# Optimization experiments

Hardware: AMD Instinct MI355X
Metric: run time of the kernel (lower is better)

## Reference

```python
import jax, jax.numpy as jnp
import numpy as np

DN = ('NCHW', 'OIHW', 'NCHW')  # data, weight, output layouts


def conv3x3(x, w):
    # stride 1, padding 1 -> spatial dims preserved (matches MyConv2d kernel_size=3, padding=1)
    return jax.lax.conv_general_dilated(
        x, w, window_strides=(1, 1), padding=((1, 1), (1, 1)), dimension_numbers=DN)


def setup_inputs() -> dict:
    key = jax.random.key(0)
    kx, k1, k2, k3 = jax.random.split(key, 4)
    N, Cin, Cmid, Cout, H, W = 16, 64, 128, 64, 224, 224
    x = jax.random.normal(kx, (N, Cin, H, W), dtype=jnp.float32)
    # Kaiming-like scaling: std = 1/sqrt(fan_in) keeps activations well-conditioned
    w1 = jax.random.normal(k1, (Cmid, Cin, 3, 3), dtype=jnp.float32) / np.sqrt(Cin * 9)
    w2 = jax.random.normal(k2, (Cmid, Cmid, 3, 3), dtype=jnp.float32) / np.sqrt(Cmid * 9)
    w3 = jax.random.normal(k3, (Cout, Cmid, 3, 3), dtype=jnp.float32) / np.sqrt(Cmid * 9)
    return {"x": x, "w1": w1, "w2": w2, "w3": w3}


def reference(x, w1, w2, w3):
    # MyNet.forward: conv1 -> conv2 -> conv3 (no bias, no activation in source)
    x = conv3x3(x, w1)
    x = conv3x3(x, w2)
    return conv3x3(x, w3)
```

## Files before the change

### kernel.cpp

```cpp
#include <hip/hip_runtime.h>
#include <hip/hip_bf16.h>

typedef __attribute__((ext_vector_type(8))) short short8;
typedef __attribute__((ext_vector_type(4))) float f32x4;
typedef __attribute__((ext_vector_type(4))) int   i32x4;
typedef __hip_bfloat16 bf16_t;

#define HH 224
#define WW 224
#define HWSZ (224*224)
#define NIMG 16

template<int CIN>
__global__ __launch_bounds__(256)
void prep_x(const float* __restrict__ x, bf16_t* __restrict__ xc) {
  constexpr int NCC = CIN/32;
  __shared__ float tile[32][225];
  int b = blockIdx.x;
  int cc = b % NCC; int h = (b/NCC) % HH; int n = b / (NCC*HH);
  const float* src = x + ((long)(n*CIN + cc*32))*HWSZ + (long)h*WW;
  for (int i = threadIdx.x; i < 32*WW; i += 256) {
    int ci = i / WW, w = i - ci*WW;
    tile[ci][w] = src[(long)ci*HWSZ + w];
  }
  __syncthreads();
  bf16_t* dst = xc + ((long)(n*HH + h)*NCC + cc)*(WW*32);
  for (int i = threadIdx.x; i < WW*32; i += 256) {
    int w = i >> 5, ci = i & 31;
    dst[i] = __float2bfloat16(tile[ci][w]);
  }
}

__global__ __launch_bounds__(256)
void prep_w(const float* __restrict__ w, bf16_t* __restrict__ wb, int Cout, int Cin) {
  int idx = blockIdx.x*256 + threadIdx.x;
  if (idx >= 9*Cout*Cin) return;
  int ci = idx % Cin; int r = idx / Cin; int co = r % Cout; int t = r / Cout;
  wb[idx] = __float2bfloat16(w[((long)co*Cin + ci)*9 + t]);
}

template<int CIN, int COUT, bool FINAL>
__global__ __launch_bounds__(256, 2)
void conv3x3(const bf16_t* __restrict__ in, const bf16_t* __restrict__ wb,
             void* __restrict__ outp)
{
  constexpr int NCC = CIN/32;
  __shared__ unsigned short lds_x[4*226*32];

  const int tid  = threadIdx.x;
  const int lane = tid & 63;
  const int l15  = lane & 15;
  const int lk   = lane >> 4;
  const int wv   = tid >> 6;
  const int rw   = wv >> 1;
  const int cb   = (wv & 1)*112;

  const int tile = blockIdx.x;
  const int n    = tile / 112;
  const int h0   = (tile - n*112)*2;
  const int co0  = blockIdx.y * 64;

  f32x4 acc[7][4];
  #pragma unroll
  for (int m=0;m<7;++m)
    #pragma unroll
    for (int q=0;q<4;++q) acc[m][q] = (f32x4){0.f,0.f,0.f,0.f};

  const bf16_t* inb   = in + (long)n * ((long)HH*NCC*WW*32);
  const bf16_t* wlane = wb + (long)(co0 + l15)*CIN + lk*8;

  for (int c = 0; c < NCC; ++c) {
    __syncthreads();
    #pragma unroll
    for (int i = 0; i < 4; ++i) {
      int hh = h0 - 1 + i;
      const char* rowp = (const char*)(inb + ((long)hh*NCC + c)*(WW*32));
      bool rowok = (hh >= 0) & (hh < HH);
      for (int off = tid*16; off < 226*64; off += 256*16) {
        int j = off >> 6;
        int wcol = j - 1;
        i32x4 v = (i32x4){0,0,0,0};
        if (rowok && (unsigned)wcol < (unsigned)WW)
          v = *(const i32x4*)(rowp + wcol*64 + (off & 63));
        int a = i*14464 + off;
        a ^= ((a>>7)&3)<<4;
        *(i32x4*)((char*)lds_x + a) = v;
      }
    }
    const bf16_t* wc = wlane + c*32;
    short8 bf[4];
    #pragma unroll
    for (int q=0;q<4;++q)
      bf[q] = *(const short8*)(wc + (long)(q*16)*CIN);
    __syncthreads();

    for (int t = 0; t < 9; ++t) {
      short8 bfn[4];
      if (t < 8) {
        #pragma unroll
        for (int q=0;q<4;++q)
          bfn[q] = *(const short8*)(wc + (long)((t+1)*COUT + q*16)*CIN);
      }
      const int dh = t/3, dw = t - (t/3)*3;
      const int arow = (rw + dh)*226;
      #pragma unroll
      for (int m=0;m<7;++m) {
        int a = (arow + cb + m*16 + l15 + dw)*64 + lk*16;
        a ^= ((a>>7)&3)<<4;
        short8 af = *(const short8*)((const char*)lds_x + a);
        #pragma unroll
        for (int q=0;q<4;++q)
          acc[m][q] = __builtin_amdgcn_mfma_f32_16x16x32_bf16(af, bf[q], acc[m][q], 0,0,0);
      }
      if (t < 8) {
        #pragma unroll
        for (int q=0;q<4;++q) bf[q] = bfn[q];
      }
    }
  }

  const int orow = h0 + rw;
  if (!FINAL) {
    bf16_t* out = (bf16_t*)outp;
    long ob = ((long)(n*HH + orow)*(COUT/32))*(WW*32);
    #pragma unroll
    for (int m=0;m<7;++m) {
      #pragma unroll
      for (int q=0;q<4;++q) {
        int co = co0 + q*16 + l15;
        long base = ob + ((long)(co>>5)*WW)*32 + (co & 31);
        int col = cb + m*16 + lk*4;
        #pragma unroll
        for (int jj=0;jj<4;++jj)
          out[base + (long)(col+jj)*32] = __float2bfloat16(acc[m][q][jj]);
      }
    }
  } else {
    float* out = (float*)outp;
    #pragma unroll
    for (int m=0;m<7;++m) {
      #pragma unroll
      for (int q=0;q<4;++q) {
        int co = co0 + q*16 + l15;
        int col = cb + m*16 + lk*4;
        *(f32x4*)(out + ((long)(n*COUT + co)*HH + orow)*WW + col) = acc[m][q];
      }
    }
  }
}

extern "C" void kernel_launch(void* const* d_in, const int* in_sizes, int n_in,
                              void* d_out, int out_size, void* d_ws, size_t ws_size,
                              hipStream_t stream) {
  (void)in_sizes; (void)n_in; (void)out_size; (void)ws_size;
  const float* x  = (const float*)d_in[0];
  const float* w1 = (const float*)d_in[1];
  const float* w2 = (const float*)d_in[2];
  const float* w3 = (const float*)d_in[3];

  const size_t SB = (size_t)NIMG*HH*WW*128*2;
  char* ws = (char*)d_ws;
  bf16_t* bufA = (bf16_t*)ws;
  bf16_t* a1   = (bf16_t*)d_out;
  bf16_t* wb1  = (bf16_t*)(ws + SB);
  bf16_t* wb2  = wb1 + 9*128*64;
  bf16_t* wb3  = wb2 + 9*128*128;

  prep_x<64><<<NIMG*HH*2, 256, 0, stream>>>(x, bufA);
  prep_w<<<(9*128*64 + 255)/256, 256, 0, stream>>>(w1, wb1, 128, 64);
  prep_w<<<(9*128*128 + 255)/256, 256, 0, stream>>>(w2, wb2, 128, 128);
  prep_w<<<(9*64*128 + 255)/256, 256, 0, stream>>>(w3, wb3, 64, 128);

  conv3x3<64,128,false><<<dim3(NIMG*112, 2), 256, 0, stream>>>(bufA, wb1, a1);
  conv3x3<128,128,false><<<dim3(NIMG*112, 2), 256, 0, stream>>>(a1, wb2, bufA);
  conv3x3<128,64,true ><<<dim3(NIMG*112, 1), 256, 0, stream>>>(bufA, wb3, (float*)d_out);
}
```

Before: 1.282 ms.

## Restructure conv tiles: per-wave output-channel split, half-width tiles, double-buffered LDS

Each workgroup now covers two output rows by 112 columns and every output channel, with one wave per 16-channel group and row. The old version split output channels across the grid and gave each wave four channel groups. The input halo for the next 32-channel chunk is loaded into registers while the current chunk computes, then written to a second LDS buffer, which removes one barrier per chunk. Block indices are also remapped in an XCD-style interleave. The intent is to load each input tile once for all output channels, raise occupancy with fewer accumulators per wave, and overlap global loads with MFMA work. The cost is larger 1024-thread blocks, weight fragments reloaded per wave, and more halo overhead at narrower tiles.

Measured after the change: 1.337 ms. 4.3% more time.

```diff
diff --git a/kernel.cpp b/kernel.cpp
--- a/kernel.cpp
+++ b/kernel.cpp
@@ -39,112 +39,123 @@
   wb[idx] = __float2bfloat16(w[((long)co*Cin + ci)*9 + t]);
 }
 
-template<int CIN, int COUT, bool FINAL>
-__global__ __launch_bounds__(256, 2)
+template<int CIN, int COUT, int T, bool FINAL>
+__global__ __launch_bounds__(T, 4)
 void conv3x3(const bf16_t* __restrict__ in, const bf16_t* __restrict__ wb,
              void* __restrict__ outp)
 {
-  constexpr int NCC = CIN/32;
-  __shared__ unsigned short lds_x[4*226*32];
+  constexpr int NCC  = CIN/32;
+  constexpr int NCOQ = COUT/16;
+  constexpr int ROWB = 114*64;
+  constexpr int BUFB = 4*ROWB;
+  constexpr int SLOTS = BUFB/16;
+  constexpr int NLD  = (SLOTS + T - 1)/T;
+  __shared__ char lds_x[2*BUFB];
 
   const int tid  = threadIdx.x;
   const int lane = tid & 63;
   const int l15  = lane & 15;
   const int lk   = lane >> 4;
   const int wv   = tid >> 6;
-  const int rw   = wv >> 1;
-  const int cb   = (wv & 1)*112;
+  const int rw   = wv / NCOQ;
+  const int coq  = wv % NCOQ;
 
-  const int tile = blockIdx.x;
-  const int n    = tile / 112;
-  const int h0   = (tile - n*112)*2;
-  const int co0  = blockIdx.y * 64;
+  constexpr int NWG = NIMG*112*2;
+  int bid = blockIdx.x;
+  int wk  = (bid & 7)*(NWG/8) + (bid >> 3);
+  const int n   = wk / 224;
+  int rem = wk - n*224;
+  const int h0  = (rem >> 1)*2;
+  const int c0  = (rem & 1)*112;
 
-  f32x4 acc[7][4];
+  f32x4 acc[7];
   #pragma unroll
-  for (int m=0;m<7;++m)
+  for (int m=0;m<7;++m) acc[m] = (f32x4){0.f,0.f,0.f,0.f};
+
+  const bf16_t* inb   = in + (long)n*HH*NCC*WW*32;
+  const bf16_t* wlane = wb + (long)(coq*16 + l15)*CIN + lk*8;
+
+  i32x4 sreg[NLD];
+
+  auto stage_load = [&](int c) {
     #pragma unroll
-    for (int q=0;q<4;++q) acc[m][q] = (f32x4){0.f,0.f,0.f,0.f};
+    for (int u=0; u<NLD; ++u) {
+      int idx = tid + u*T;
+      sreg[u] = (i32x4){0,0,0,0};
+      if (idx < SLOTS) {
+        int i = idx/456; int r456 = idx - i*456;
+        int j = r456 >> 2; int q = r456 & 3;
+        int hh = h0 - 1 + i;
+        int icol = c0 + j - 1;
+        if ((unsigned)hh < (unsigned)HH && (unsigned)icol < (unsigned)WW) {
+          const char* p = (const char*)(inb + (((long)hh*NCC + c)*WW + icol)*32) + q*16;
+          sreg[u] = *(const i32x4*)p;
+        }
+      }
+    }
+  };
+  auto stage_write = [&](char* buf) {
+    #pragma unroll
+    for (int u=0; u<NLD; ++u) {
+      int idx = tid + u*T;
+      if (idx < SLOTS) {
+        int a = idx*16;
+        a ^= ((a>>7)&3)<<4;
+        *(i32x4*)(buf + a) = sreg[u];
+      }
+    }
+  };
 
-  const bf16_t* inb   = in + (long)n * ((long)HH*NCC*WW*32);
-  const bf16_t* wlane = wb + (long)(co0 + l15)*CIN + lk*8;
+  stage_load(0);
+  stage_write(lds_x);
+  __syncthreads();
+  int cur = 0;
 
   for (int c = 0; c < NCC; ++c) {
-    __syncthreads();
+    if (c+1 < NCC) stage_load(c+1);
+    const bf16_t* wc = wlane + c*32;
+    const char* buf = lds_x + cur*BUFB;
+    short8 bf = *(const short8*)wc;
     #pragma unroll
-    for (int i = 0; i < 4; ++i) {
-      int hh = h0 - 1 + i;
-      const char* rowp = (const char*)(inb + ((long)hh*NCC + c)*(WW*32));
-      bool rowok = (hh >= 0) & (hh < HH);
-      for (int off = tid*16; off < 226*64; off += 256*16) {
-        int j = off >> 6;
-        int wcol = j - 1;
-        i32x4 v = (i32x4){0,0,0,0};
-        if (rowok && (unsigned)wcol < (unsigned)WW)
-          v = *(const i32x4*)(rowp + wcol*64 + (off & 63));
-        int a = i*14464 + off;
-        a ^= ((a>>7)&3)<<4;
-        *(i32x4*)((char*)lds_x + a) = v;
-      }
-    }
-    const bf16_t* wc = wlane + c*32;
-    short8 bf[4];
-    #pragma unroll
-    for (int q=0;q<4;++q)
-      bf[q] = *(const short8*)(wc + (long)(q*16)*CIN);
-    __syncthreads();
-
-    for (int t = 0; t < 9; ++t) {
-      short8 bfn[4];
-      if (t < 8) {
-        #pragma unroll
-        for (int q=0;q<4;++q)
-          bfn[q] = *(const short8*)(wc + (long)((t+1)*COUT + q*16)*CIN);
-      }
-      const int dh = t/3, dw = t - (t/3)*3;
-      const int arow = (rw + dh)*226;
+    for (int t=0; t<9; ++t) {
+      short8 bfn;
+      if (t<8) bfn = *(const short8*)(wc + (long)(t+1)*COUT*CIN);
+      int dh = t/3, dw = t - dh*3;
+      int arow = (rw+dh)*ROWB;
       #pragma unroll
       for (int m=0;m<7;++m) {
-        int a = (arow + cb + m*16 + l15 + dw)*64 + lk*16;
+        int a = arow + (m*16 + l15 + dw)*64 + lk*16;
         a ^= ((a>>7)&3)<<4;
-        short8 af = *(const short8*)((const char*)lds_x + a);
-        #pragma unroll
-        for (int q=0;q<4;++q)
-          acc[m][q] = __builtin_amdgcn_mfma_f32_16x16x32_bf16(af, bf[q], acc[m][q], 0,0,0);
+        short8 af = *(const short8*)(buf + a);
+        acc[m] = __builtin_amdgcn_mfma_f32_16x16x32_bf16(af, bf, acc[m], 0,0,0);
       }
-      if (t < 8) {
-        #pragma unroll
-        for (int q=0;q<4;++q) bf[q] = bfn[q];
-      }
+      if (t<8) bf = bfn;
     }
+    if (c+1 < NCC) stage_write(lds_x + (cur^1)*BUFB);
+    __syncthreads();
+    cur ^= 1;
   }
 
   const int orow = h0 + rw;
+  const int co   = coq*16 + l15;
   if (!FINAL) {
     bf16_t* out = (bf16_t*)outp;
-    long ob = ((long)(n*HH + orow)*(COUT/32))*(WW*32);
+    constexpr int NCO = COUT/32;
+    long ob = (((long)n*HH + orow)*NCO + (co>>5))*((long)WW*32) + (co&31);
     #pragma unroll
     for (int m=0;m<7;++m) {
+      int col = c0 + m*16 + lk*4;
       #pragma unroll
-      for (int q=0;q<4;++q) {
-        int co = co0 + q*16 + l15;
-        long base = ob + ((long)(co>>5)*WW)*32 + (co & 31);
-        int col = cb + m*16 + lk*4;
-        #pragma unroll
-        for (int jj=0;jj<4;++jj)
-          out[base + (long)(col+jj)*32] = __float2bfloat16(acc[m][q][jj]);
-      }
+      for (int jj=0;jj<4;++jj)
+        out[ob + (long)(col+jj)*32] = __float2bfloat16(acc[m][jj]);
     }
   } else {
     float* out = (float*)outp;
+    long ob = (((long)n*COUT + co)*HH + orow)*(long)WW;
     #pragma unroll
     for (int m=0;m<7;++m) {
-      #pragma unroll
-      for (int q=0;q<4;++q) {
-        int co = co0 + q*16 + l15;
-        int col = cb + m*16 + lk*4;
-        *(f32x4*)(out + ((long)(n*COUT + co)*HH + orow)*WW + col) = acc[m][q];
-      }
+      int col = c0 + m*16 + lk*4;
+      *(f32x4*)(out + ob + col) = acc[m];
     }
   }
 }
@@ -171,7 +182,7 @@
   prep_w<<<(9*128*128 + 255)/256, 256, 0, stream>>>(w2, wb2, 128, 128);
   prep_w<<<(9*64*128 + 255)/256, 256, 0, stream>>>(w3, wb3, 64, 128);
 
-  conv3x3<64,128,false><<<dim3(NIMG*112, 2), 256, 0, stream>>>(bufA, wb1, a1);
-  conv3x3<128,128,false><<<dim3(NIMG*112, 2), 256, 0, stream>>>(a1, wb2, bufA);
-  conv3x3<128,64,true ><<<dim3(NIMG*112, 1), 256, 0, stream>>>(bufA, wb3, (float*)d_out);
+  conv3x3<64,128,1024,false><<<NIMG*112*2, 1024, 0, stream>>>(bufA, wb1, a1);
+  conv3x3<128,128,1024,false><<<NIMG*112*2, 1024, 0, stream>>>(a1, wb2, bufA);
+  conv3x3<128,64,512,true ><<<NIMG*112*2, 512, 0, stream>>>(bufA, wb3, (float*)d_out);
 }
```
